# Performance work log

Hardware: AMD Instinct MI355X
Metric: run time of the kernel (lower is better)

Reference implementation:

```python
import jax, jax.numpy as jnp
import numpy as np

TH_HIGH = 0.6
TH_LOW = 0.3
NEGPOS_RATIO = 3
VAR0, VAR1 = 0.1, 0.2
IMG_SIZE = 255.0


def point_form(a):
    # (cx,cy,w,h) -> (xmin,ymin,xmax,ymax)
    return jnp.concatenate([a[..., :2] - a[..., 2:] / 2,
                            a[..., :2] + a[..., 2:] / 2], axis=-1)


def jaccard(a, b):
    # a: [B,4] point form, b: [A,4] point form -> IoU [B,A]
    lt = jnp.maximum(a[:, None, :2], b[None, :, :2])
    rb = jnp.minimum(a[:, None, 2:], b[None, :, 2:])
    wh = jnp.clip(rb - lt, 0.0)
    inter = wh[..., 0] * wh[..., 1]
    area_a = ((a[:, 2] - a[:, 0]) * (a[:, 3] - a[:, 1]))[:, None]
    area_b = ((b[:, 2] - b[:, 0]) * (b[:, 3] - b[:, 1]))[None, :]
    return inter / (area_a + area_b - inter)


def encode(matched, priors):
    # matched: point form, priors: center-size form (standard SSD encode)
    g_cxcy = ((matched[..., :2] + matched[..., 2:]) / 2 - priors[..., :2]) / (VAR0 * priors[..., 2:])
    g_wh = jnp.log((matched[..., 2:] - matched[..., :2]) / priors[..., 2:]) / VAR1
    return jnp.concatenate([g_cxcy, g_wh], axis=-1)


def decode(loc, priors):
    # standard SSD decode -> point form boxes
    cxcy = priors[..., :2] + loc[..., :2] * VAR0 * priors[..., 2:]
    wh = priors[..., 2:] * jnp.exp(loc[..., 2:] * VAR1)
    mins = cxcy - wh / 2
    return jnp.concatenate([mins, mins + wh], axis=-1)


def smooth_l1(x):
    ax = jnp.abs(x)
    return jnp.where(ax < 1.0, 0.5 * x * x, ax - 0.5)


def setup_inputs() -> dict:
    key = jax.random.key(0)
    k1, k2, k3, k4 = jax.random.split(key, 4)
    B, G, S = 64, 128, 4
    A = G * G * S  # 65536 anchors
    c = (jnp.arange(G, dtype=jnp.float32) + 0.5) / G
    cxcy = jnp.stack(jnp.meshgrid(c, c, indexing='ij'), axis=-1).reshape(-1, 2)  # [G*G,2]
    scales = jnp.array([0.08, 0.12, 0.2, 0.3], dtype=jnp.float32)
    wh = jnp.stack([scales, scales], axis=-1)  # [S,2]
    anchors = jnp.concatenate([jnp.repeat(cxcy, S, axis=0), jnp.tile(wh, (G * G, 1))], axis=-1)  # [A,4] center-size
    # gt boxes: small jitter around a random anchor so positives exist
    idx = jax.random.randint(k1, (B,), 0, A)
    gt_cs = anchors[idx] * (1.0 + 0.03 * jax.random.normal(k2, (B, 4), dtype=jnp.float32))
    gt_boxes = point_form(gt_cs)  # [B,4] point form
    loc_pred = 0.5 * jax.random.normal(k3, (B, A, 4), dtype=jnp.float32)
    conf_pred = jax.random.normal(k4, (B, A, 2), dtype=jnp.float32)
    return {"loc_pred": loc_pred, "conf_pred": conf_pred, "gt_boxes": gt_boxes, "anchors": anchors}


def reference(loc_pred, conf_pred, gt_boxes, anchors):
    B, A, _ = loc_pred.shape
    pf_anchors = point_form(anchors)
    overlaps = jaccard(gt_boxes, pf_anchors)                      # [B,A]
    labels = (overlaps >= TH_HIGH).astype(jnp.int32) - \
             ((overlaps > TH_LOW) & (overlaps < TH_HIGH)).astype(jnp.int32)
    pos = labels == 1                                             # [B,A]
    neg0 = labels == 0
    N = pos.sum()
    Nf = jnp.maximum(N.astype(loc_pred.dtype), 1.0)

    loc_gt = encode(gt_boxes[:, None, :], anchors[None, :, :])    # [B,A,4]
    elem = smooth_l1(loc_pred - loc_gt)
    loss_loc = (elem * pos[..., None]).sum() / (Nf * 4.0)

    # --- hard negative mining ---
    logp = jax.nn.log_softmax(conf_pred, axis=-1)                 # [B,A,2]
    tgt = pos.astype(jnp.int32)
    nll = -jnp.take_along_axis(logp, tgt[..., None], axis=-1)[..., 0]  # [B,A]
    ce = jnp.where(neg0, nll, 0.0)
    loss_idx = jnp.argsort(-ce, axis=1)                           # descending
    idx_rank = jnp.argsort(loss_idx, axis=1)
    num_pos = pos.sum(axis=1, keepdims=True)
    num_neg = jnp.clip(NEGPOS_RATIO * num_pos, 10, A - 1)
    neg = idx_rank < num_neg                                      # [B,A]

    # --- weighted classification loss over picked pos+neg ---
    sel = pos | neg
    w = jnp.array([1.0 / 3.0, 1.0], dtype=conf_pred.dtype)
    wsel = jnp.where(sel, w[tgt], 0.0)
    loss_cls = (nll * wsel).sum() / wsel.sum()

    # --- accuracies on picked set ---
    pred_cls = jnp.argmax(conf_pred, axis=-1)
    pos_m = sel & (tgt == 1)
    neg_m = sel & (tgt == 0)
    pos_accuracy = ((pred_cls == 1) & pos_m).sum() / jnp.maximum(pos_m.sum(), 1)
    neg_accuracy = ((pred_cls == 0) & neg_m).sum() / jnp.maximum(neg_m.sum(), 1)

    # --- decoded diagnostics (masked means over positives) ---
    decoded = decode(loc_pred, anchors[None, :, :])               # [B,A,4] point form
    pos_err = jnp.linalg.norm((gt_boxes[:, None, :2] - decoded[..., :2]) * IMG_SIZE, axis=-1)
    position_error = (pos_err * pos).sum() / Nf
    size_diff = jnp.abs(gt_boxes[:, None, 2:] - decoded[..., 2:])  # [B,A,2]
    size_errors = (size_diff * pos[..., None]).sum(axis=(0, 1)) / Nf * IMG_SIZE

    return (loss_loc, loss_cls, pos_accuracy, neg_accuracy, position_error, size_errors, N)
```

## Files before the change

kernel.cpp:

```cpp
#include <hip/hip_runtime.h>
#include <math.h>


#define MAXB 64
#define NSLOT 1024
#define NB 2048
#define CHUNKS 4

struct Accum {
  float f_loc[NSLOT], f_clsp[NSLOT], f_perr[NSLOT], f_se0[NSLOT], f_se1[NSLOT];
  int i_pcor[NSLOT], i_pcnt[NSLOT];
  float f_clsn_row[MAXB];
  unsigned int i_ntot_row[MAXB], i_ncor_row[MAXB];
  float sc_cls[MAXB][CHUNKS];
  int sc_ncnt[MAXB][CHUNKS], sc_ncor[MAXB][CHUNKS];
  unsigned int sc_ccnt[MAXB][CHUNKS];
  unsigned int tstar[MAXB], rrank[MAXB];
  unsigned int done;
};

__device__ __forceinline__ float iou_f(float4 g, float4 an) {
  float ax0 = an.x - an.z * 0.5f, ay0 = an.y - an.w * 0.5f;
  float ax1 = an.x + an.z * 0.5f, ay1 = an.y + an.w * 0.5f;
  float ltx = fmaxf(g.x, ax0), lty = fmaxf(g.y, ay0);
  float rbx = fminf(g.z, ax1), rby = fminf(g.w, ay1);
  float w = fmaxf(rbx - ltx, 0.f), h = fmaxf(rby - lty, 0.f);
  float inter = w * h;
  float area_g = (g.z - g.x) * (g.w - g.y);
  float area_a = (ax1 - ax0) * (ay1 - ay0);
  return inter / (area_g + area_a - inter);
}

__device__ __forceinline__ float sl1(float x) {
  float ax = fabsf(x);
  return ax < 1.f ? 0.5f * x * x : ax - 0.5f;
}

__global__ __launch_bounds__(256) void k_main(
    const float* __restrict__ loc_pred, const float* __restrict__ conf,
    const float* __restrict__ gt, const float* __restrict__ anchors,
    Accum* __restrict__ acc, unsigned int* __restrict__ g1c,
    unsigned int* __restrict__ keys, int A) {
  int b = blockIdx.y;
  int tid = threadIdx.x;
  int lane = tid & 63, wv = tid >> 6;
  __shared__ unsigned int hist[4][NB];
  __shared__ float smf[5][4];
  __shared__ int smi[2][4];
  for (int i = tid; i < 4 * NB; i += 256) ((unsigned int*)hist)[i] = 0u;
  __syncthreads();

  float4 g4 = reinterpret_cast<const float4*>(gt)[b];
  const float4* conf4 = reinterpret_cast<const float4*>(conf);
  const float4* anc4 = reinterpret_cast<const float4*>(anchors);
  const float4* loc4 = reinterpret_cast<const float4*>(loc_pred);
  int abase = blockIdx.x * 4096;
  long long cbase = ((long long)b * A + abase) >> 1;
  uint2* keys2 = reinterpret_cast<uint2*>(keys);

  float loc_s = 0.f, clsp = 0.f, perr = 0.f, se0 = 0.f, se1 = 0.f;
  int pcnt = 0, pcor = 0;

#pragma unroll
  for (int j = 0; j < 8; ++j) {
    float4 cc = conf4[cbase + tid + j * 256];
    int a0 = abase + 2 * (tid + j * 256);
    uint2 kv;
#pragma unroll
    for (int h = 0; h < 2; ++h) {
      int a = a0 + h;
      float c0 = h ? cc.z : cc.x;
      float c1 = h ? cc.w : cc.y;
      float4 an = anc4[a];
      float ov = iou_f(g4, an);
      float s = logf(1.0f + expf(-fabsf(c1 - c0)));
      float m = fmaxf(c0, c1);
      unsigned int kk = 0u;
      if (ov <= 0.3f) kk = __float_as_uint((m - c0) + s);
      if (c1 > c0) kk |= 0x80000000u;
      if (h) kv.y = kk; else kv.x = kk;
      atomicAdd(&hist[wv][(kk & 0x7FFFFFFFu) >> 20], 1u);
      if (ov >= 0.6f) {
        float4 lp = loc4[(long long)b * A + a];
        float gcx = (g4.x + g4.z) * 0.5f, gcy = (g4.y + g4.w) * 0.5f;
        float gw = g4.z - g4.x, gh = g4.w - g4.y;
        float t0 = (gcx - an.x) / (0.1f * an.z);
        float t1 = (gcy - an.y) / (0.1f * an.w);
        float t2 = logf(gw / an.z) / 0.2f;
        float t3 = logf(gh / an.w) / 0.2f;
        loc_s += sl1(lp.x - t0) + sl1(lp.y - t1) + sl1(lp.z - t2) +
                 sl1(lp.w - t3);
        clsp += (m - c1) + s;
        pcnt += 1;
        pcor += (c1 > c0) ? 1 : 0;
        float dcx = an.x + lp.x * 0.1f * an.z;
        float dcy = an.y + lp.y * 0.1f * an.w;
        float dw = an.z * expf(lp.z * 0.2f);
        float dh = an.w * expf(lp.w * 0.2f);
        float dx0 = dcx - dw * 0.5f, dy0 = dcy - dh * 0.5f;
        float ex = (g4.x - dx0) * 255.f, ey = (g4.y - dy0) * 255.f;
        perr += sqrtf(ex * ex + ey * ey);
        se0 += fabsf(g4.z - (dx0 + dw));
        se1 += fabsf(g4.w - (dy0 + dh));
      }
    }
    keys2[cbase + tid + j * 256] = kv;
  }

  float fv[5] = {loc_s, clsp, perr, se0, se1};
  int iv[2] = {pcnt, pcor};
#pragma unroll
  for (int q = 0; q < 5; ++q) {
    float v = fv[q];
#pragma unroll
    for (int o = 32; o > 0; o >>= 1) v += __shfl_down(v, o, 64);
    if (lane == 0) smf[q][wv] = v;
  }
#pragma unroll
  for (int q = 0; q < 2; ++q) {
    int v = iv[q];
#pragma unroll
    for (int o = 32; o > 0; o >>= 1) v += __shfl_down(v, o, 64);
    if (lane == 0) smi[q][wv] = v;
  }
  __syncthreads();

  {
    int slot = b * gridDim.x + blockIdx.x;
    unsigned int* dst = g1c + (long long)slot * NB;
    for (int i = tid; i < NB; i += 256)
      dst[i] = hist[0][i] + hist[1][i] + hist[2][i] + hist[3][i];
  }

  if (tid == 0) {
    float L = 0, C = 0, P = 0, S0 = 0, S1 = 0;
    int PC = 0, COR = 0;
    for (int w2 = 0; w2 < 4; ++w2) {
      L += smf[0][w2]; C += smf[1][w2]; P += smf[2][w2];
      S0 += smf[3][w2]; S1 += smf[4][w2];
      PC += smi[0][w2]; COR += smi[1][w2];
    }
    int slot = b * gridDim.x + blockIdx.x;
    acc->f_loc[slot] = L;
    acc->f_clsp[slot] = C;
    acc->f_perr[slot] = P;
    acc->f_se0[slot] = S0;
    acc->f_se1[slot] = S1;
    acc->i_pcor[slot] = COR;
    acc->i_pcnt[slot] = PC;
    if (slot == 0) acc->done = 0u;
  }
}

template <int PER>
__device__ uint2 pickR(const unsigned int* cnt, int kr, unsigned int* s_wsum,
                       volatile unsigned int* s_bin,
                       volatile unsigned int* s_kr) {
  const int tid = threadIdx.x, lane = tid & 63, wv = tid >> 6;
  unsigned int my = 0;
#pragma unroll
  for (int i = 0; i < PER; ++i) my += cnt[i];
  unsigned int v = my;
#pragma unroll
  for (int o = 1; o < 64; o <<= 1) {
    unsigned int tv = __shfl_down(v, o, 64);
    if (lane + o < 64) v += tv;
  }
  if (lane == 0) s_wsum[wv] = v;
  __syncthreads();
  unsigned int off = 0;
#pragma unroll
  for (int w2 = 0; w2 < 16; ++w2)
    if (w2 > wv) off += s_wsum[w2];
  unsigned int incl = v + off;
  unsigned int above = incl - my;
  if ((int)above < kr && kr <= (int)incl) {
    int kk = kr - (int)above;
#pragma unroll
    for (int i = PER - 1; i >= 0; --i) {
      int c = (int)cnt[i];
      if (kk <= c) {
        *s_bin = (unsigned int)(tid * PER + i);
        *s_kr = (unsigned int)kk;
        break;
      }
      kk -= c;
    }
  }
  __syncthreads();
  uint2 r;
  r.x = *s_bin;
  r.y = *s_kr;
  __syncthreads();
  return r;
}

template <int PER>
__device__ uint2 pick4(const unsigned int* cnt, int kr, unsigned int* s_wsum,
                       volatile unsigned int* s_bin,
                       volatile unsigned int* s_kr) {
  const int tid = threadIdx.x, lane = tid & 63, wv = tid >> 6;
  unsigned int my = 0;
#pragma unroll
  for (int i = 0; i < PER; ++i) my += cnt[i];
  unsigned int v = my;
#pragma unroll
  for (int o = 1; o < 64; o <<= 1) {
    unsigned int tv = __shfl_down(v, o, 64);
    if (lane + o < 64) v += tv;
  }
  if (lane == 0) s_wsum[wv] = v;
  __syncthreads();
  unsigned int off = 0;
#pragma unroll
  for (int w2 = 0; w2 < 4; ++w2)
    if (w2 > wv) off += s_wsum[w2];
  unsigned int incl = v + off;
  unsigned int above = incl - my;
  if ((int)above < kr && kr <= (int)incl) {
    int kk = kr - (int)above;
#pragma unroll
    for (int i = PER - 1; i >= 0; --i) {
      int c = (int)cnt[i];
      if (kk <= c) {
        *s_bin = (unsigned int)(tid * PER + i);
        *s_kr = (unsigned int)kk;
        break;
      }
      kk -= c;
    }
  }
  __syncthreads();
  uint2 r;
  r.x = *s_bin;
  r.y = *s_kr;
  __syncthreads();
  return r;
}

__device__ __forceinline__ float bredf16(float v, float* s) {
#pragma unroll
  for (int o = 32; o > 0; o >>= 1) v += __shfl_down(v, o, 64);
  int lane = threadIdx.x & 63, wv = threadIdx.x >> 6;
  if (lane == 0) s[wv] = v;
  __syncthreads();
  float r = 0;
#pragma unroll
  for (int w = 0; w < 16; ++w) r += s[w];
  __syncthreads();
  return r;
}

__device__ __forceinline__ int bredi16(int v, int* s) {
#pragma unroll
  for (int o = 32; o > 0; o >>= 1) v += __shfl_down(v, o, 64);
  int lane = threadIdx.x & 63, wv = threadIdx.x >> 6;
  if (lane == 0) s[wv] = v;
  __syncthreads();
  int r = 0;
#pragma unroll
  for (int w = 0; w < 16; ++w) r += s[w];
  __syncthreads();
  return r;
}

__device__ __forceinline__ float bredf4(float v, float* s) {
#pragma unroll
  for (int o = 32; o > 0; o >>= 1) v += __shfl_down(v, o, 64);
  int lane = threadIdx.x & 63, wv = threadIdx.x >> 6;
  if (lane == 0) s[wv] = v;
  __syncthreads();
  float r = s[0] + s[1] + s[2] + s[3];
  __syncthreads();
  return r;
}

__device__ __forceinline__ int bredi4(int v, int* s) {
#pragma unroll
  for (int o = 32; o > 0; o >>= 1) v += __shfl_down(v, o, 64);
  int lane = threadIdx.x & 63, wv = threadIdx.x >> 6;
  if (lane == 0) s[wv] = v;
  __syncthreads();
  int r = s[0] + s[1] + s[2] + s[3];
  __syncthreads();
  return r;
}

__global__ __launch_bounds__(1024) void k_scan(
    const unsigned int* __restrict__ keys, const unsigned int* __restrict__ g1c,
    Accum* __restrict__ acc, unsigned int* __restrict__ cand, int A, int spr) {
  int b = blockIdx.y;
  int c = blockIdx.x;
  int tid = threadIdx.x;
  int lane = tid & 63;
  __shared__ unsigned int s_wsum[16];
  __shared__ volatile unsigned int s_bin, s_kr;
  __shared__ int s_np[16];
  __shared__ unsigned int s_ccnt;
  __shared__ float s_f[16];
  __shared__ int s_i[16];

  unsigned int cnt2[2] = {0u, 0u};
  {
    const uint2* pc =
        reinterpret_cast<const uint2*>(g1c + (long long)b * spr * NB);
    for (int s = 0; s < spr; ++s) {
      uint2 p = pc[s * (NB / 2) + tid];
      cnt2[0] += p.x;
      cnt2[1] += p.y;
    }
  }
  if (tid < spr) s_np[tid] = acc->i_pcnt[b * spr + tid];
  if (tid == 0) s_ccnt = 0u;
  __syncthreads();

  int np = 0;
  for (int i = 0; i < spr; ++i) np += s_np[i];
  int k = 3 * np;
  if (k < 10) k = 10;
  if (k > A - 1) k = A - 1;

  uint2 p1 = pickR<2>(cnt2, k, s_wsum, &s_bin, &s_kr);
  unsigned int tstar = p1.x;
  int r = (int)p1.y;
  if (c == 0 && tid == 0) {
    acc->tstar[b] = tstar;
    acc->rrank[b] = (unsigned int)r;
  }

  int ck = A / CHUNKS;
  const uint4* k4 = reinterpret_cast<const uint4*>(keys);
  long long base4 = (((long long)b * A) >> 2) + (long long)c * (ck >> 2);
  unsigned int* crow = cand + (long long)b * A + (long long)c * ck;
  float cls = 0.f;
  int ncnt = 0, ncor = 0;
  uint4 v[4];
#pragma unroll
  for (int j = 0; j < 4; ++j) v[j] = k4[base4 + tid + j * 1024];
#pragma unroll
  for (int j = 0; j < 4; ++j) {
    unsigned int ks[4] = {v[j].x, v[j].y, v[j].z, v[j].w};
#pragma unroll
    for (int e = 0; e < 4; ++e) {
      unsigned int key = ks[e];
      unsigned int k31 = key & 0x7FFFFFFFu;
      unsigned int vp = k31 >> 20;
      if (vp > tstar) {
        cls += __uint_as_float(k31);
        ncnt += 1;
        ncor += (int)((key >> 31) ^ 1u);
      }
      bool inb = (vp == tstar);
      unsigned long long mb = __ballot(inb);
      if (mb) {
        int leader = __ffsll((unsigned long long)mb) - 1;
        unsigned int base = 0;
        if (lane == leader)
          base = atomicAdd(&s_ccnt, (unsigned int)__popcll(mb));
        base = __shfl(base, leader, 64);
        if (inb) crow[base + __popcll(mb & ((1ull << lane) - 1ull))] = key;
      }
    }
  }

  float C = bredf16(cls, s_f);
  int NC = bredi16(ncnt, s_i);
  int CR = bredi16(ncor, s_i);
  if (tid == 0) {
    acc->sc_cls[b][c] = C;
    acc->sc_ncnt[b][c] = NC;
    acc->sc_ncor[b][c] = CR;
    acc->sc_ccnt[b][c] = s_ccnt;
  }
}

__global__ __launch_bounds__(256) void k_fin(
    const unsigned int* __restrict__ cand, Accum* __restrict__ acc,
    float* __restrict__ out, int A, int spr) {
  int b = blockIdx.x;
  int tid = threadIdx.x;
  __shared__ unsigned int hist2[1024];
  __shared__ unsigned int s_wsum[4];
  __shared__ volatile unsigned int s_bin, s_kr;
  __shared__ unsigned int s_eq, s_last;
  __shared__ float s_f[4];
  __shared__ int s_i[4];

  unsigned int tstar = acc->tstar[b];
  int r = (int)acc->rrank[b];
  int ck = A / CHUNKS;
  unsigned int cc[CHUNKS];
#pragma unroll
  for (int c = 0; c < CHUNKS; ++c) cc[c] = acc->sc_ccnt[b][c];
  const unsigned int* crow = cand + (long long)b * A;
  if (tid == 0) s_eq = 0u;

  for (int i = tid; i < 1024; i += 256) hist2[i] = 0u;
  __syncthreads();
#pragma unroll
  for (int c = 0; c < CHUNKS; ++c)
    for (unsigned int i = tid; i < cc[c]; i += 256)
      atomicAdd(&hist2[(crow[c * ck + i] >> 10) & 0x3FFu], 1u);
  __syncthreads();
  unsigned int cl[4];
#pragma unroll
  for (int i = 0; i < 4; ++i) cl[i] = hist2[tid * 4 + i];
  uint2 p2 = pick4<4>(cl, r, s_wsum, &s_bin, &s_kr);
  r = (int)p2.y;

  for (int i = tid; i < 1024; i += 256) hist2[i] = 0u;
  __syncthreads();
#pragma unroll
  for (int c = 0; c < CHUNKS; ++c)
    for (unsigned int i = tid; i < cc[c]; i += 256) {
      unsigned int k31 = crow[c * ck + i] & 0x7FFFFFFFu;
      if (((k31 >> 10) & 0x3FFu) == p2.x) atomicAdd(&hist2[k31 & 0x3FFu], 1u);
    }
  __syncthreads();
#pragma unroll
  for (int i = 0; i < 4; ++i) cl[i] = hist2[tid * 4 + i];
  uint2 p3 = pick4<4>(cl, r, s_wsum, &s_bin, &s_kr);
  unsigned int thr = (tstar << 20) | (p2.x << 10) | p3.x;
  int need = (int)p3.y;

  float cls = 0.f;
  int ncnt = 0, ncor = 0;
#pragma unroll
  for (int c = 0; c < CHUNKS; ++c)
    for (unsigned int i = tid; i < cc[c]; i += 256) {
      unsigned int key = crow[c * ck + i];
      unsigned int k31 = key & 0x7FFFFFFFu;
      bool s = false;
      if (k31 > thr) {
        s = true;
      } else if (k31 == thr) {
        unsigned int ord = atomicAdd(&s_eq, 1u);
        if ((int)ord < need) s = true;
      }
      if (s) {
        cls += __uint_as_float(k31);
        ncnt += 1;
        ncor += (int)((key >> 31) ^ 1u);
      }
    }
  float C = bredf4(cls, s_f);
  int NC = bredi4(ncnt, s_i);
  int CR = bredi4(ncor, s_i);
  if (tid == 0) {
    float c0 = 0;
    int n0 = 0, r0 = 0;
    for (int c = 0; c < CHUNKS; ++c) {
      c0 += acc->sc_cls[b][c];
      n0 += acc->sc_ncnt[b][c];
      r0 += acc->sc_ncor[b][c];
    }
    acc->f_clsn_row[b] = C + c0;
    acc->i_ntot_row[b] = (unsigned int)(NC + n0);
    acc->i_ncor_row[b] = (unsigned int)(CR + r0);
  }

  __threadfence();
  if (tid == 0) {
    unsigned int old = __hip_atomic_fetch_add(&acc->done, 1u, __ATOMIC_ACQ_REL,
                                              __HIP_MEMORY_SCOPE_AGENT);
    s_last = (old == (unsigned int)(gridDim.x - 1)) ? 1u : 0u;
  }
  __syncthreads();
  if (!s_last) return;
  __threadfence();

  int B = (int)gridDim.x;
  int nslot = spr * B;
  float F0 = 0, F1 = 0, F2 = 0, F3 = 0, F4 = 0, F5 = 0;
  int I0 = 0, I1 = 0, I2 = 0, I3 = 0;
  for (int i = tid; i < nslot; i += 256) {
    F0 += acc->f_loc[i];
    F1 += acc->f_clsp[i];
    F2 += acc->f_perr[i];
    F3 += acc->f_se0[i];
    F4 += acc->f_se1[i];
    I0 += acc->i_pcor[i];
    I1 += acc->i_pcnt[i];
  }
  for (int i = tid; i < B; i += 256) {
    F5 += acc->f_clsn_row[i];
    I2 += (int)acc->i_ntot_row[i];
    I3 += (int)acc->i_ncor_row[i];
  }
  float T0 = bredf4(F0, s_f);
  float T1 = bredf4(F1, s_f);
  float T2 = bredf4(F2, s_f);
  float T3 = bredf4(F3, s_f);
  float T4 = bredf4(F4, s_f);
  float T5 = bredf4(F5, s_f);
  int P0 = bredi4(I0, s_i);
  int P1 = bredi4(I1, s_i);
  int P2 = bredi4(I2, s_i);
  int P3 = bredi4(I3, s_i);

  if (tid == 0) {
    float N = (float)P1;
    float Nf = fmaxf(N, 1.f);
    out[0] = T0 / (Nf * 4.f);
    float wsum = N + (float)P2 * (1.f / 3.f);
    out[1] = (T1 + T5 * (1.f / 3.f)) / wsum;
    out[2] = (float)P0 / fmaxf(N, 1.f);
    out[3] = (float)P3 / fmaxf((float)P2, 1.f);
    out[4] = T2 / Nf;
    out[5] = T3 / Nf * 255.f;
    out[6] = T4 / Nf * 255.f;
    out[7] = N;
  }
}

extern "C" void kernel_launch(void* const* d_in, const int* in_sizes, int n_in,
                              void* d_out, int out_size, void* d_ws,
                              size_t ws_size, hipStream_t stream) {
  (void)n_in; (void)out_size; (void)ws_size;
  const float* loc = (const float*)d_in[0];
  const float* conf = (const float*)d_in[1];
  const float* gt = (const float*)d_in[2];
  const float* anchors = (const float*)d_in[3];
  int B = in_sizes[2] / 4;
  int A = in_sizes[3] / 4;
  float* out = (float*)d_out;

  int spr = A / 4096;

  char* w = (char*)d_ws;
  Accum* acc = (Accum*)w;
  size_t off = (sizeof(Accum) + 255) & ~(size_t)255;
  unsigned int* g1c = (unsigned int*)(w + off);
  off += (size_t)B * spr * NB * 4;
  off = (off + 255) & ~(size_t)255;
  unsigned int* keys = (unsigned int*)(w + off);
  off += (size_t)B * A * 4;
  unsigned int* cand = (unsigned int*)(w + off);

  dim3 gmain(spr, B);
  k_main<<<gmain, 256, 0, stream>>>(loc, conf, gt, anchors, acc, g1c, keys, A);
  dim3 gscan(CHUNKS, B);
  k_scan<<<gscan, 1024, 0, stream>>>(keys, g1c, acc, cand, A, spr);
  k_fin<<<B, 256, 0, stream>>>(cand, acc, out, A, spr);
}
```

Before: 155.8 us.

## Pack per-block histograms into 16-bit pairs and widen final kernel to 1024 threads

The main kernel now keeps two shared histogram replicas instead of four and writes per-block histograms as packed 16-bit pairs. This halves the global histogram traffic between the main and scan kernels, and the scan kernel gets a fully unrolled path for the common slot count. The final selection kernel runs 1024 threads, with one histogram bin per thread and 16-wave reductions. Fewer replicas may raise atomic contention in shared memory, and the 16-bit counts rely on each block holding at most 4096 entries.

New measurement: 173.2 us. +11.2%, slower.

```diff
diff --git a/kernel.cpp b/kernel.cpp
--- a/kernel.cpp
+++ b/kernel.cpp
@@ -5,6 +5,7 @@
 #define MAXB 64
 #define NSLOT 1024
 #define NB 2048
+#define NBP 1024
 #define CHUNKS 4
 
 struct Accum {
@@ -39,15 +40,15 @@
 __global__ __launch_bounds__(256) void k_main(
     const float* __restrict__ loc_pred, const float* __restrict__ conf,
     const float* __restrict__ gt, const float* __restrict__ anchors,
-    Accum* __restrict__ acc, unsigned int* __restrict__ g1c,
+    Accum* __restrict__ acc, unsigned int* __restrict__ g1p,
     unsigned int* __restrict__ keys, int A) {
   int b = blockIdx.y;
   int tid = threadIdx.x;
   int lane = tid & 63, wv = tid >> 6;
-  __shared__ unsigned int hist[4][NB];
+  __shared__ unsigned int hist[2][NB];
   __shared__ float smf[5][4];
   __shared__ int smi[2][4];
-  for (int i = tid; i < 4 * NB; i += 256) ((unsigned int*)hist)[i] = 0u;
+  for (int i = tid; i < 2 * NB; i += 256) ((unsigned int*)hist)[i] = 0u;
   __syncthreads();
 
   float4 g4 = reinterpret_cast<const float4*>(gt)[b];
@@ -57,6 +58,7 @@
   int abase = blockIdx.x * 4096;
   long long cbase = ((long long)b * A + abase) >> 1;
   uint2* keys2 = reinterpret_cast<uint2*>(keys);
+  unsigned int* hrep = hist[wv >> 1];
 
   float loc_s = 0.f, clsp = 0.f, perr = 0.f, se0 = 0.f, se1 = 0.f;
   int pcnt = 0, pcor = 0;
@@ -79,7 +81,7 @@
       if (ov <= 0.3f) kk = __float_as_uint((m - c0) + s);
       if (c1 > c0) kk |= 0x80000000u;
       if (h) kv.y = kk; else kv.x = kk;
-      atomicAdd(&hist[wv][(kk & 0x7FFFFFFFu) >> 20], 1u);
+      atomicAdd(&hrep[(kk & 0x7FFFFFFFu) >> 20], 1u);
       if (ov >= 0.6f) {
         float4 lp = loc4[(long long)b * A + a];
         float gcx = (g4.x + g4.z) * 0.5f, gcy = (g4.y + g4.w) * 0.5f;
@@ -127,9 +129,12 @@
 
   {
     int slot = b * gridDim.x + blockIdx.x;
-    unsigned int* dst = g1c + (long long)slot * NB;
-    for (int i = tid; i < NB; i += 256)
-      dst[i] = hist[0][i] + hist[1][i] + hist[2][i] + hist[3][i];
+    unsigned int* dst = g1p + (long long)slot * NBP;
+    for (int i = tid; i < NBP; i += 256) {
+      unsigned int lo = hist[0][2 * i] + hist[1][2 * i];
+      unsigned int hi = hist[0][2 * i + 1] + hist[1][2 * i + 1];
+      dst[i] = lo | (hi << 16);
+    }
   }
 
   if (tid == 0) {
@@ -195,49 +200,6 @@
   return r;
 }
 
-template <int PER>
-__device__ uint2 pick4(const unsigned int* cnt, int kr, unsigned int* s_wsum,
-                       volatile unsigned int* s_bin,
-                       volatile unsigned int* s_kr) {
-  const int tid = threadIdx.x, lane = tid & 63, wv = tid >> 6;
-  unsigned int my = 0;
-#pragma unroll
-  for (int i = 0; i < PER; ++i) my += cnt[i];
-  unsigned int v = my;
-#pragma unroll
-  for (int o = 1; o < 64; o <<= 1) {
-    unsigned int tv = __shfl_down(v, o, 64);
-    if (lane + o < 64) v += tv;
-  }
-  if (lane == 0) s_wsum[wv] = v;
-  __syncthreads();
-  unsigned int off = 0;
-#pragma unroll
-  for (int w2 = 0; w2 < 4; ++w2)
-    if (w2 > wv) off += s_wsum[w2];
-  unsigned int incl = v + off;
-  unsigned int above = incl - my;
-  if ((int)above < kr && kr <= (int)incl) {
-    int kk = kr - (int)above;
-#pragma unroll
-    for (int i = PER - 1; i >= 0; --i) {
-      int c = (int)cnt[i];
-      if (kk <= c) {
-        *s_bin = (unsigned int)(tid * PER + i);
-        *s_kr = (unsigned int)kk;
-        break;
-      }
-      kk -= c;
-    }
-  }
-  __syncthreads();
-  uint2 r;
-  r.x = *s_bin;
-  r.y = *s_kr;
-  __syncthreads();
-  return r;
-}
-
 __device__ __forceinline__ float bredf16(float v, float* s) {
 #pragma unroll
   for (int o = 32; o > 0; o >>= 1) v += __shfl_down(v, o, 64);
@@ -264,30 +226,8 @@
   return r;
 }
 
-__device__ __forceinline__ float bredf4(float v, float* s) {
-#pragma unroll
-  for (int o = 32; o > 0; o >>= 1) v += __shfl_down(v, o, 64);
-  int lane = threadIdx.x & 63, wv = threadIdx.x >> 6;
-  if (lane == 0) s[wv] = v;
-  __syncthreads();
-  float r = s[0] + s[1] + s[2] + s[3];
-  __syncthreads();
-  return r;
-}
-
-__device__ __forceinline__ int bredi4(int v, int* s) {
-#pragma unroll
-  for (int o = 32; o > 0; o >>= 1) v += __shfl_down(v, o, 64);
-  int lane = threadIdx.x & 63, wv = threadIdx.x >> 6;
-  if (lane == 0) s[wv] = v;
-  __syncthreads();
-  int r = s[0] + s[1] + s[2] + s[3];
-  __syncthreads();
-  return r;
-}
-
 __global__ __launch_bounds__(1024) void k_scan(
-    const unsigned int* __restrict__ keys, const unsigned int* __restrict__ g1c,
+    const unsigned int* __restrict__ keys, const unsigned int* __restrict__ g1p,
     Accum* __restrict__ acc, unsigned int* __restrict__ cand, int A, int spr) {
   int b = blockIdx.y;
   int c = blockIdx.x;
@@ -302,12 +242,20 @@
 
   unsigned int cnt2[2] = {0u, 0u};
   {
-    const uint2* pc =
-        reinterpret_cast<const uint2*>(g1c + (long long)b * spr * NB);
-    for (int s = 0; s < spr; ++s) {
-      uint2 p = pc[s * (NB / 2) + tid];
-      cnt2[0] += p.x;
-      cnt2[1] += p.y;
+    const unsigned int* pc = g1p + (long long)b * spr * NBP + tid;
+    if (spr == 16) {
+#pragma unroll
+      for (int s = 0; s < 16; ++s) {
+        unsigned int p = pc[s * NBP];
+        cnt2[0] += p & 0xFFFFu;
+        cnt2[1] += p >> 16;
+      }
+    } else {
+      for (int s = 0; s < spr; ++s) {
+        unsigned int p = pc[s * NBP];
+        cnt2[0] += p & 0xFFFFu;
+        cnt2[1] += p >> 16;
+      }
     }
   }
   if (tid < spr) s_np[tid] = acc->i_pcnt[b * spr + tid];
@@ -374,17 +322,17 @@
   }
 }
 
-__global__ __launch_bounds__(256) void k_fin(
+__global__ __launch_bounds__(1024) void k_fin(
     const unsigned int* __restrict__ cand, Accum* __restrict__ acc,
     float* __restrict__ out, int A, int spr) {
   int b = blockIdx.x;
   int tid = threadIdx.x;
   __shared__ unsigned int hist2[1024];
-  __shared__ unsigned int s_wsum[4];
+  __shared__ unsigned int s_wsum[16];
   __shared__ volatile unsigned int s_bin, s_kr;
   __shared__ unsigned int s_eq, s_last;
-  __shared__ float s_f[4];
-  __shared__ int s_i[4];
+  __shared__ float s_f[16];
+  __shared__ int s_i[16];
 
   unsigned int tstar = acc->tstar[b];
   int r = (int)acc->rrank[b];
@@ -395,31 +343,28 @@
   const unsigned int* crow = cand + (long long)b * A;
   if (tid == 0) s_eq = 0u;
 
-  for (int i = tid; i < 1024; i += 256) hist2[i] = 0u;
+  hist2[tid] = 0u;
   __syncthreads();
 #pragma unroll
   for (int c = 0; c < CHUNKS; ++c)
-    for (unsigned int i = tid; i < cc[c]; i += 256)
+    for (unsigned int i = tid; i < cc[c]; i += 1024)
       atomicAdd(&hist2[(crow[c * ck + i] >> 10) & 0x3FFu], 1u);
   __syncthreads();
-  unsigned int cl[4];
-#pragma unroll
-  for (int i = 0; i < 4; ++i) cl[i] = hist2[tid * 4 + i];
-  uint2 p2 = pick4<4>(cl, r, s_wsum, &s_bin, &s_kr);
+  unsigned int c1 = hist2[tid];
+  uint2 p2 = pickR<1>(&c1, r, s_wsum, &s_bin, &s_kr);
   r = (int)p2.y;
 
-  for (int i = tid; i < 1024; i += 256) hist2[i] = 0u;
+  hist2[tid] = 0u;
   __syncthreads();
 #pragma unroll
   for (int c = 0; c < CHUNKS; ++c)
-    for (unsigned int i = tid; i < cc[c]; i += 256) {
+    for (unsigned int i = tid; i < cc[c]; i += 1024) {
       unsigned int k31 = crow[c * ck + i] & 0x7FFFFFFFu;
       if (((k31 >> 10) & 0x3FFu) == p2.x) atomicAdd(&hist2[k31 & 0x3FFu], 1u);
     }
   __syncthreads();
-#pragma unroll
-  for (int i = 0; i < 4; ++i) cl[i] = hist2[tid * 4 + i];
-  uint2 p3 = pick4<4>(cl, r, s_wsum, &s_bin, &s_kr);
+  unsigned int c2 = hist2[tid];
+  uint2 p3 = pickR<1>(&c2, r, s_wsum, &s_bin, &s_kr);
   unsigned int thr = (tstar << 20) | (p2.x << 10) | p3.x;
   int need = (int)p3.y;
 
@@ -427,7 +372,7 @@
   int ncnt = 0, ncor = 0;
 #pragma unroll
   for (int c = 0; c < CHUNKS; ++c)
-    for (unsigned int i = tid; i < cc[c]; i += 256) {
+    for (unsigned int i = tid; i < cc[c]; i += 1024) {
       unsigned int key = crow[c * ck + i];
       unsigned int k31 = key & 0x7FFFFFFFu;
       bool s = false;
@@ -443,9 +388,9 @@
         ncor += (int)((key >> 31) ^ 1u);
       }
     }
-  float C = bredf4(cls, s_f);
-  int NC = bredi4(ncnt, s_i);
-  int CR = bredi4(ncor, s_i);
+  float C = bredf16(cls, s_f);
+  int NC = bredi16(ncnt, s_i);
+  int CR = bredi16(ncor, s_i);
   if (tid == 0) {
     float c0 = 0;
     int n0 = 0, r0 = 0;
@@ -473,7 +418,7 @@
   int nslot = spr * B;
   float F0 = 0, F1 = 0, F2 = 0, F3 = 0, F4 = 0, F5 = 0;
   int I0 = 0, I1 = 0, I2 = 0, I3 = 0;
-  for (int i = tid; i < nslot; i += 256) {
+  for (int i = tid; i < nslot; i += 1024) {
     F0 += acc->f_loc[i];
     F1 += acc->f_clsp[i];
     F2 += acc->f_perr[i];
@@ -482,21 +427,21 @@
     I0 += acc->i_pcor[i];
     I1 += acc->i_pcnt[i];
   }
-  for (int i = tid; i < B; i += 256) {
+  for (int i = tid; i < B; i += 1024) {
     F5 += acc->f_clsn_row[i];
     I2 += (int)acc->i_ntot_row[i];
     I3 += (int)acc->i_ncor_row[i];
   }
-  float T0 = bredf4(F0, s_f);
-  float T1 = bredf4(F1, s_f);
-  float T2 = bredf4(F2, s_f);
-  float T3 = bredf4(F3, s_f);
-  float T4 = bredf4(F4, s_f);
-  float T5 = bredf4(F5, s_f);
-  int P0 = bredi4(I0, s_i);
-  int P1 = bredi4(I1, s_i);
-  int P2 = bredi4(I2, s_i);
-  int P3 = bredi4(I3, s_i);
+  float T0 = bredf16(F0, s_f);
+  float T1 = bredf16(F1, s_f);
+  float T2 = bredf16(F2, s_f);
+  float T3 = bredf16(F3, s_f);
+  float T4 = bredf16(F4, s_f);
+  float T5 = bredf16(F5, s_f);
+  int P0 = bredi16(I0, s_i);
+  int P1 = bredi16(I1, s_i);
+  int P2 = bredi16(I2, s_i);
+  int P3 = bredi16(I3, s_i);
 
   if (tid == 0) {
     float N = (float)P1;
@@ -530,16 +475,16 @@
   char* w = (char*)d_ws;
   Accum* acc = (Accum*)w;
   size_t off = (sizeof(Accum) + 255) & ~(size_t)255;
-  unsigned int* g1c = (unsigned int*)(w + off);
-  off += (size_t)B * spr * NB * 4;
+  unsigned int* g1p = (unsigned int*)(w + off);
+  off += (size_t)B * spr * NBP * 4;
   off = (off + 255) & ~(size_t)255;
   unsigned int* keys = (unsigned int*)(w + off);
   off += (size_t)B * A * 4;
   unsigned int* cand = (unsigned int*)(w + off);
 
   dim3 gmain(spr, B);
-  k_main<<<gmain, 256, 0, stream>>>(loc, conf, gt, anchors, acc, g1c, keys, A);
+  k_main<<<gmain, 256, 0, stream>>>(loc, conf, gt, anchors, acc, g1p, keys, A);
   dim3 gscan(CHUNKS, B);
-  k_scan<<<gscan, 1024, 0, stream>>>(keys, g1c, acc, cand, A, spr);
-  k_fin<<<B, 256, 0, stream>>>(cand, acc, out, A, spr);
-}
+  k_scan<<<gscan, 1024, 0, stream>>>(keys, g1p, acc, cand, A, spr);
+  k_fin<<<B, 1024, 0, stream>>>(cand, acc, out, A, spr);
+}
```

## Pack per-block histograms into 16-bit pairs and split final reduction into separate kernel

Applied to the files above, without the earlier changes.

Per-block 2048-bin histograms are now written as packed pairs of 16-bit counts, halving the partial-histogram traffic between k_main and k_scan, and k_scan gets an unrolled path for the common 16-slot case. The last-block-done atomic counter and its fences in k_fin are removed, and the global reduction moves into a new single-block k_out launch. This trades the atomic and fence cost for one extra kernel launch. Packing assumes each bin count per 4096-anchor block fits in 16 bits, which holds since a block has at most 4096 elements.

New measurement: 146.6 us. -5.9%, faster.

```diff
diff --git a/kernel.cpp b/kernel.cpp
--- a/kernel.cpp
+++ b/kernel.cpp
@@ -5,6 +5,7 @@
 #define MAXB 64
 #define NSLOT 1024
 #define NB 2048
+#define NBP 1024
 #define CHUNKS 4
 
 struct Accum {
@@ -16,7 +17,6 @@
   int sc_ncnt[MAXB][CHUNKS], sc_ncor[MAXB][CHUNKS];
   unsigned int sc_ccnt[MAXB][CHUNKS];
   unsigned int tstar[MAXB], rrank[MAXB];
-  unsigned int done;
 };
 
 __device__ __forceinline__ float iou_f(float4 g, float4 an) {
@@ -39,7 +39,7 @@
 __global__ __launch_bounds__(256) void k_main(
     const float* __restrict__ loc_pred, const float* __restrict__ conf,
     const float* __restrict__ gt, const float* __restrict__ anchors,
-    Accum* __restrict__ acc, unsigned int* __restrict__ g1c,
+    Accum* __restrict__ acc, unsigned int* __restrict__ g1p,
     unsigned int* __restrict__ keys, int A) {
   int b = blockIdx.y;
   int tid = threadIdx.x;
@@ -57,6 +57,7 @@
   int abase = blockIdx.x * 4096;
   long long cbase = ((long long)b * A + abase) >> 1;
   uint2* keys2 = reinterpret_cast<uint2*>(keys);
+  unsigned int* hrep = hist[wv];
 
   float loc_s = 0.f, clsp = 0.f, perr = 0.f, se0 = 0.f, se1 = 0.f;
   int pcnt = 0, pcor = 0;
@@ -79,7 +80,7 @@
       if (ov <= 0.3f) kk = __float_as_uint((m - c0) + s);
       if (c1 > c0) kk |= 0x80000000u;
       if (h) kv.y = kk; else kv.x = kk;
-      atomicAdd(&hist[wv][(kk & 0x7FFFFFFFu) >> 20], 1u);
+      atomicAdd(&hrep[(kk & 0x7FFFFFFFu) >> 20], 1u);
       if (ov >= 0.6f) {
         float4 lp = loc4[(long long)b * A + a];
         float gcx = (g4.x + g4.z) * 0.5f, gcy = (g4.y + g4.w) * 0.5f;
@@ -127,9 +128,14 @@
 
   {
     int slot = b * gridDim.x + blockIdx.x;
-    unsigned int* dst = g1c + (long long)slot * NB;
-    for (int i = tid; i < NB; i += 256)
-      dst[i] = hist[0][i] + hist[1][i] + hist[2][i] + hist[3][i];
+    unsigned int* dst = g1p + (long long)slot * NBP;
+    for (int i = tid; i < NBP; i += 256) {
+      unsigned int lo =
+          hist[0][2 * i] + hist[1][2 * i] + hist[2][2 * i] + hist[3][2 * i];
+      unsigned int hi = hist[0][2 * i + 1] + hist[1][2 * i + 1] +
+                        hist[2][2 * i + 1] + hist[3][2 * i + 1];
+      dst[i] = lo | (hi << 16);
+    }
   }
 
   if (tid == 0) {
@@ -148,7 +154,6 @@
     acc->f_se1[slot] = S1;
     acc->i_pcor[slot] = COR;
     acc->i_pcnt[slot] = PC;
-    if (slot == 0) acc->done = 0u;
   }
 }
 
@@ -287,7 +292,7 @@
 }
 
 __global__ __launch_bounds__(1024) void k_scan(
-    const unsigned int* __restrict__ keys, const unsigned int* __restrict__ g1c,
+    const unsigned int* __restrict__ keys, const unsigned int* __restrict__ g1p,
     Accum* __restrict__ acc, unsigned int* __restrict__ cand, int A, int spr) {
   int b = blockIdx.y;
   int c = blockIdx.x;
@@ -302,12 +307,20 @@
 
   unsigned int cnt2[2] = {0u, 0u};
   {
-    const uint2* pc =
-        reinterpret_cast<const uint2*>(g1c + (long long)b * spr * NB);
-    for (int s = 0; s < spr; ++s) {
-      uint2 p = pc[s * (NB / 2) + tid];
-      cnt2[0] += p.x;
-      cnt2[1] += p.y;
+    const unsigned int* pc = g1p + (long long)b * spr * NBP + tid;
+    if (spr == 16) {
+#pragma unroll
+      for (int s = 0; s < 16; ++s) {
+        unsigned int p = pc[s * NBP];
+        cnt2[0] += p & 0xFFFFu;
+        cnt2[1] += p >> 16;
+      }
+    } else {
+      for (int s = 0; s < spr; ++s) {
+        unsigned int p = pc[s * NBP];
+        cnt2[0] += p & 0xFFFFu;
+        cnt2[1] += p >> 16;
+      }
     }
   }
   if (tid < spr) s_np[tid] = acc->i_pcnt[b * spr + tid];
@@ -375,14 +388,13 @@
 }
 
 __global__ __launch_bounds__(256) void k_fin(
-    const unsigned int* __restrict__ cand, Accum* __restrict__ acc,
-    float* __restrict__ out, int A, int spr) {
+    const unsigned int* __restrict__ cand, Accum* __restrict__ acc, int A) {
   int b = blockIdx.x;
   int tid = threadIdx.x;
   __shared__ unsigned int hist2[1024];
   __shared__ unsigned int s_wsum[4];
   __shared__ volatile unsigned int s_bin, s_kr;
-  __shared__ unsigned int s_eq, s_last;
+  __shared__ unsigned int s_eq;
   __shared__ float s_f[4];
   __shared__ int s_i[4];
 
@@ -458,18 +470,14 @@
     acc->i_ntot_row[b] = (unsigned int)(NC + n0);
     acc->i_ncor_row[b] = (unsigned int)(CR + r0);
   }
-
-  __threadfence();
-  if (tid == 0) {
-    unsigned int old = __hip_atomic_fetch_add(&acc->done, 1u, __ATOMIC_ACQ_REL,
-                                              __HIP_MEMORY_SCOPE_AGENT);
-    s_last = (old == (unsigned int)(gridDim.x - 1)) ? 1u : 0u;
-  }
-  __syncthreads();
-  if (!s_last) return;
-  __threadfence();
-
-  int B = (int)gridDim.x;
+}
+
+__global__ __launch_bounds__(256) void k_out(const Accum* __restrict__ acc,
+                                             float* __restrict__ out, int B,
+                                             int spr) {
+  int tid = threadIdx.x;
+  __shared__ float s_f[4];
+  __shared__ int s_i[4];
   int nslot = spr * B;
   float F0 = 0, F1 = 0, F2 = 0, F3 = 0, F4 = 0, F5 = 0;
   int I0 = 0, I1 = 0, I2 = 0, I3 = 0;
@@ -530,16 +538,17 @@
   char* w = (char*)d_ws;
   Accum* acc = (Accum*)w;
   size_t off = (sizeof(Accum) + 255) & ~(size_t)255;
-  unsigned int* g1c = (unsigned int*)(w + off);
-  off += (size_t)B * spr * NB * 4;
+  unsigned int* g1p = (unsigned int*)(w + off);
+  off += (size_t)B * spr * NBP * 4;
   off = (off + 255) & ~(size_t)255;
   unsigned int* keys = (unsigned int*)(w + off);
   off += (size_t)B * A * 4;
   unsigned int* cand = (unsigned int*)(w + off);
 
   dim3 gmain(spr, B);
-  k_main<<<gmain, 256, 0, stream>>>(loc, conf, gt, anchors, acc, g1c, keys, A);
+  k_main<<<gmain, 256, 0, stream>>>(loc, conf, gt, anchors, acc, g1p, keys, A);
   dim3 gscan(CHUNKS, B);
-  k_scan<<<gscan, 1024, 0, stream>>>(keys, g1c, acc, cand, A, spr);
-  k_fin<<<B, 256, 0, stream>>>(cand, acc, out, A, spr);
-}
+  k_scan<<<gscan, 1024, 0, stream>>>(keys, g1p, acc, cand, A, spr);
+  k_fin<<<B, 256, 0, stream>>>(cand, acc, A);
+  k_out<<<1, 256, 0, stream>>>(acc, out, B, spr);
+}
```
